# Optimization experiments

Hardware: AMD Instinct MI355X
Metric: run time of the kernel (lower is better)

Reference implementation:

```python
import jax, jax.numpy as jnp
import numpy as np
from jax import lax

BETA = 0.5        # Sinkhron beta
N_ITER = 20       # got_iteration
THRESH = 0.1      # P > 0.1 threshold
NL_I = 5          # apply_non_linearity(..., 'elu', i=5)
EPS = 1e-9


def setup_inputs() -> dict:
    key = jax.random.key(0)
    k1, k2 = jax.random.split(key)
    B, N, D = 128, 512, 128
    h = jax.random.normal(k1, (B, N, D), dtype=jnp.float32)
    W0 = jnp.ones((D,), dtype=jnp.float32)
    W1 = jnp.ones((D,), dtype=jnp.float32)
    lengths = jax.random.randint(k2, (B,), 0, N, dtype=jnp.int32)
    return {"h": h, "W0": W0, "W1": W1, "lengths": lengths}


def _forward(h, W0, W1, lengths):
    B, N, D = h.shape
    lengths = jnp.maximum(lengths, 1)
    mask = (jnp.arange(N)[None, :] < lengths[:, None])          # [B, N] bool
    mf = mask.astype(h.dtype)
    mask2 = mf[:, :, None] * mf[:, None, :]                      # [B, N, N]

    # internal_forward: Diag layers with relu between (mlp_act='relu')
    h = h * W0
    h = jax.nn.relu(h)
    h = h * W1

    # cost_matrix_batch_torch: cosine similarity, add identity diag, mask
    hn = h / (jnp.linalg.norm(h, axis=-1, keepdims=True) + 1e-12)
    sim = jnp.einsum('bnd,bmd->bnm', hn, hn)                     # [B, N, N]
    sim = sim + jnp.eye(N, dtype=h.dtype)                        # add_eye_diag
    sim = sim * mask2
    cost = (1.0 - sim) * mask2

    # Sinkhorn with uniform marginals on valid nodes, fixed iterations
    n = lengths.astype(h.dtype)
    mu = mf / n[:, None]                                         # [B, N]
    K = jnp.exp(-cost / BETA) * mask2                            # [B, N, N]

    def body(carry, _):
        u, v = carry
        u = mu / (jnp.einsum('bnm,bm->bn', K, v) + EPS) * mf
        v = mu / (jnp.einsum('bnm,bn->bm', K, u) + EPS) * mf
        return (u, v), None

    (u, v), _ = lax.scan(body, (mf, mf), None, length=N_ITER)
    P = u[:, :, None] * K * v[:, None, :]                        # transport plan

    # P.detach(); scale by number of nodes per graph; threshold
    P = lax.stop_gradient(P)
    P = n[:, None, None] * P
    A = (P > THRESH).astype(h.dtype)
    similarity = A * sim
    # apply_non_linearity 'elu': elu(x*i - i) + 1
    out = jax.nn.elu(similarity * NL_I - NL_I) + 1.0
    return out


def reference(h, W0, W1, lengths):
    return _forward(h, W0, W1, lengths)
```

## Files before the change

kernel.cpp:

```cpp
#include <hip/hip_runtime.h>

#define BB 128
#define NN 512
#define DD 128

__global__ __launch_bounds__(256) void hn_kernel(const float* __restrict__ h,
                                                 const float* __restrict__ W0,
                                                 const float* __restrict__ W1,
                                                 float* __restrict__ hn) {
    int wave = (int)((blockIdx.x * blockDim.x + threadIdx.x) >> 6);
    int lane = threadIdx.x & 63;
    const float2* h2 = (const float2*)(h + (size_t)wave * DD);
    float2 w0 = ((const float2*)W0)[lane];
    float2 w1 = ((const float2*)W1)[lane];
    float2 x = h2[lane];
    float p0 = fmaxf(x.x * w0.x, 0.0f) * w1.x;
    float p1 = fmaxf(x.y * w0.y, 0.0f) * w1.y;
    float ss = p0 * p0 + p1 * p1;
#pragma unroll
    for (int m = 32; m; m >>= 1) ss += __shfl_xor(ss, m);
    float inv = 1.0f / (sqrtf(ss) + 1e-12f);
    float2 o;
    o.x = p0 * inv;
    o.y = p1 * inv;
    ((float2*)(hn + (size_t)wave * DD))[lane] = o;
}

#define KC 32
__global__ __launch_bounds__(256) void sim_kernel(const float* __restrict__ hn,
                                                  const int* __restrict__ lengths,
                                                  float* __restrict__ K) {
    __shared__ float As[KC][132];
    __shared__ float Bs[KC][132];
    __shared__ int pre[BB + 1];
    int tid = threadIdx.x;
    if (tid == 0) {
        int acc = 0;
        for (int b = 0; b < BB; b++) {
            pre[b] = acc;
            int len = max(lengths[b], 1);
            int nt = (len + 127) >> 7;
            acc += nt * nt;
        }
        pre[BB] = acc;
    }
    __syncthreads();
    int total = pre[BB];

    int lr = tid >> 3;
    int lk = (tid & 7) << 2;
    int tx = tid & 15, ty = tid >> 4;

    for (int t = blockIdx.x; t < total; t += gridDim.x) {
        int lo = 0, hi = BB;
        while (lo + 1 < hi) {
            int mid = (lo + hi) >> 1;
            if (pre[mid] <= t) lo = mid; else hi = mid;
        }
        int b = lo;
        int local = t - pre[b];
        int len = max(lengths[b], 1);
        int nt = (len + 127) >> 7;
        int ti = local / nt;
        int tj = local - ti * nt;
        int r0 = ti << 7, c0 = tj << 7;
        const float* base = hn + (size_t)b * NN * DD;
        float acc[8][8] = {};

        for (int kc = 0; kc < DD; kc += KC) {
#pragma unroll
            for (int rr = 0; rr < 128; rr += 32) {
                float4 a = *(const float4*)(base + (size_t)(r0 + lr + rr) * DD + kc + lk);
                As[lk + 0][lr + rr] = a.x; As[lk + 1][lr + rr] = a.y;
                As[lk + 2][lr + rr] = a.z; As[lk + 3][lr + rr] = a.w;
                float4 bb = *(const float4*)(base + (size_t)(c0 + lr + rr) * DD + kc + lk);
                Bs[lk + 0][lr + rr] = bb.x; Bs[lk + 1][lr + rr] = bb.y;
                Bs[lk + 2][lr + rr] = bb.z; Bs[lk + 3][lr + rr] = bb.w;
            }
            __syncthreads();
#pragma unroll
            for (int kk = 0; kk < KC; kk++) {
                float4 a0 = *(const float4*)&As[kk][ty * 8];
                float4 a1 = *(const float4*)&As[kk][ty * 8 + 4];
                float4 b0 = *(const float4*)&Bs[kk][tx * 4];
                float4 b1 = *(const float4*)&Bs[kk][64 + tx * 4];
                float ar[8] = {a0.x, a0.y, a0.z, a0.w, a1.x, a1.y, a1.z, a1.w};
                float bc[8] = {b0.x, b0.y, b0.z, b0.w, b1.x, b1.y, b1.z, b1.w};
#pragma unroll
                for (int r = 0; r < 8; r++)
#pragma unroll
                    for (int c = 0; c < 8; c++)
                        acc[r][c] = fmaf(ar[r], bc[c], acc[r][c]);
            }
            __syncthreads();
        }
        float* out = K + (size_t)b * NN * NN;
#pragma unroll
        for (int r = 0; r < 8; r++) {
            int i = r0 + ty * 8 + r;
            if (i >= len) continue;
#pragma unroll
            for (int cg = 0; cg < 2; cg++) {
                int j0 = c0 + cg * 64 + tx * 4;
                if (j0 >= len) continue;
                float vv[4];
#pragma unroll
                for (int c = 0; c < 4; c++) {
                    float s = acc[r][cg * 4 + c] + ((i == j0 + c) ? 1.0f : 0.0f);
                    vv[c] = expf(2.0f * s - 2.0f);
                }
                float4 o;
                o.x = vv[0]; o.y = vv[1]; o.z = vv[2]; o.w = vv[3];
                *(float4*)(out + (size_t)i * NN + j0) = o;
            }
        }
    }
}

__device__ __forceinline__ float dot8(float4 A, float4 B, float4 x0, float4 x1) {
    float d = fmaf(A.x, x0.x, fmaf(A.y, x0.y, fmaf(A.z, x0.z, A.w * x0.w)));
    return fmaf(B.x, x1.x, fmaf(B.y, x1.y, fmaf(B.z, x1.z, fmaf(B.w, x1.w, d))));
}

#define ROWS22(X) X(0) X(1) X(2) X(3) X(4) X(5) X(6) X(7) X(8) X(9) X(10) \
    X(11) X(12) X(13) X(14) X(15) X(16) X(17) X(18) X(19) X(20) X(21)

__global__ __launch_bounds__(512, 2) void coop_sink(const float* __restrict__ K,
                                                    float* __restrict__ u_buf,
                                                    float* __restrict__ v_buf,
                                                    const int* __restrict__ lengths,
                                                    unsigned long long* __restrict__ slots64) {
    __shared__ float xb[NN];
    __shared__ float pv[8 * NN];
    __shared__ int Sh[BB], Pre[BB];

    int g = blockIdx.x;
    int tid = threadIdx.x;

    if (tid == 0) {
        int need[BB]; int ssum = 0;
        for (int m = 0; m < BB; m++) {
            int L = max(lengths[m], 1);
            need[m] = (L + 175) / 176;
            ssum += need[m];
        }
        while (ssum > 256) {
            int best = 0, bv = need[0];
            for (int m = 1; m < BB; m++)
                if (need[m] > bv) { bv = need[m]; best = m; }
            need[best]--; ssum--;
        }
        int acc = 0;
        for (int m = 0; m < BB; m++) { Pre[m] = acc; Sh[m] = need[m]; acc += need[m]; }
    }
    __syncthreads();

    int m = -1;
    for (int mm = 0; mm < BB; mm++)
        if (g >= Pre[mm] && g < Pre[mm] + Sh[mm]) { m = mm; break; }
    if (m < 0) return;
    int b = m;
    int jbase = Pre[m];
    int q = g - jbase;
    int S = Sh[m];

    int len = max(lengths[b], 1);
    int len4 = (len + 3) & ~3;
    int rpq = (len + S - 1) / S;
    int r_lo = q * rpq;
    int nrows = min(len - r_lo, rpq);
    if (nrows < 0) nrows = 0;
    float inv_n = 1.0f / (float)len;

    int w = tid >> 6, l = tid & 63;
    int c0 = 4 * l, c1 = 256 + 4 * l;
    bool a0 = c0 < len4, a1 = c1 < len4;
    const float* Kb = K + (size_t)b * NN * NN;

    xb[tid] = (tid < len) ? 1.0f : 0.0f;

#define DECL(o) float4 kA##o = {0,0,0,0}, kB##o = {0,0,0,0};
    ROWS22(DECL)
#undef DECL
#define FILL_ROW(o)                                                          \
    {                                                                        \
        int i_ = w + 8 * (o);                                                \
        if (i_ < nrows) {                                                    \
            const float* g0_ = Kb + (size_t)(r_lo + i_) * NN;                \
            if (a0) kA##o = *(const float4*)(g0_ + c0);                      \
            if (a1) kB##o = *(const float4*)(g0_ + c1);                      \
        }                                                                    \
    }
    ROWS22(FILL_ROW)
#undef FILL_ROW

    __syncthreads();

    for (int t = 0; t < 20; t++) {
        float4 xv0 = *(const float4*)(xb + c0);
        float4 xv1 = *(const float4*)(xb + c1);
        float4 pa = {0, 0, 0, 0}, pb = {0, 0, 0, 0};

#define DOT(o) float d##o = dot8(kA##o, kB##o, xv0, xv1);
        ROWS22(DOT)
#undef DOT
#pragma unroll
        for (int mm2 = 32; mm2; mm2 >>= 1) {
#define BF(o) d##o += __shfl_xor(d##o, mm2);
            ROWS22(BF)
#undef BF
        }
#define RC(o) float uu##o = inv_n / (d##o + 1e-9f);
        ROWS22(RC)
#undef RC
#define ACC_ROW(o)                                                           \
    pa.x = fmaf(kA##o.x, uu##o, pa.x); pa.y = fmaf(kA##o.y, uu##o, pa.y);    \
    pa.z = fmaf(kA##o.z, uu##o, pa.z); pa.w = fmaf(kA##o.w, uu##o, pa.w);    \
    pb.x = fmaf(kB##o.x, uu##o, pb.x); pb.y = fmaf(kB##o.y, uu##o, pb.y);    \
    pb.z = fmaf(kB##o.z, uu##o, pb.z); pb.w = fmaf(kB##o.w, uu##o, pb.w);
        ROWS22(ACC_ROW)
#undef ACC_ROW
        if (t == 19 && l == 0) {
            float* ub = u_buf + (size_t)b * NN + r_lo + w;
#define ST(o) if (w + 8 * (o) < nrows) ub[8 * (o)] = uu##o;
            ROWS22(ST)
#undef ST
        }

        for (int i = 176 + w; i < nrows; i += 8) {
            const float* g0 = Kb + (size_t)(r_lo + i) * NN;
            float4 A = {0, 0, 0, 0}, B = {0, 0, 0, 0};
            if (a0) A = *(const float4*)(g0 + c0);
            if (a1) B = *(const float4*)(g0 + c1);
            float d = dot8(A, B, xv0, xv1);
#pragma unroll
            for (int mm2 = 32; mm2; mm2 >>= 1) d += __shfl_xor(d, mm2);
            float uu = inv_n / (d + 1e-9f);
            pa.x = fmaf(A.x, uu, pa.x); pa.y = fmaf(A.y, uu, pa.y);
            pa.z = fmaf(A.z, uu, pa.z); pa.w = fmaf(A.w, uu, pa.w);
            pb.x = fmaf(B.x, uu, pb.x); pb.y = fmaf(B.y, uu, pb.y);
            pb.z = fmaf(B.z, uu, pb.z); pb.w = fmaf(B.w, uu, pb.w);
            if (t == 19 && l == 0) u_buf[(size_t)b * NN + r_lo + i] = uu;
        }

        *(float4*)(pv + w * NN + c0) = pa;
        *(float4*)(pv + w * NN + c1) = pb;
        __syncthreads();
        int c = tid;
        float s0 = pv[c] + pv[NN + c] + pv[2 * NN + c] + pv[3 * NN + c] +
                   pv[4 * NN + c] + pv[5 * NN + c] + pv[6 * NN + c] + pv[7 * NN + c];
        unsigned long long* pbase =
            slots64 + ((size_t)(t & 1) * 512) * 512;
        if (S > 1) {
            unsigned long long pk =
                ((unsigned long long)(unsigned)(t + 1) << 32) | __float_as_uint(s0);
            __hip_atomic_store(pbase + (size_t)g * 512 + c, pk,
                               __ATOMIC_RELAXED, __HIP_MEMORY_SCOPE_AGENT);
        }

        float t0 = s0;
        for (int s = 1; s < S; s++) {
            int k = q + s; if (k >= S) k -= S;
            const unsigned long long* p64 = pbase + (size_t)(jbase + k) * 512 + c;
            unsigned long long vpk =
                __hip_atomic_load(p64, __ATOMIC_RELAXED, __HIP_MEMORY_SCOPE_AGENT);
            while ((unsigned)(vpk >> 32) != (unsigned)(t + 1)) {
                __builtin_amdgcn_s_sleep(1);
                vpk = __hip_atomic_load(p64, __ATOMIC_RELAXED, __HIP_MEMORY_SCOPE_AGENT);
            }
            t0 += __uint_as_float((unsigned)vpk);
        }
        float v0 = (c < len) ? (inv_n / (t0 + 1e-9f)) : 0.0f;
        if (t < 19) {
            xb[c] = v0;
        } else if (c >= r_lo && c < r_lo + nrows) {
            v_buf[(size_t)b * NN + c] = v0;
        }
        __syncthreads();
    }
}

__global__ __launch_bounds__(256) void epi_kernel(float* __restrict__ io,
                                                  const float* __restrict__ u,
                                                  const float* __restrict__ v,
                                                  const int* __restrict__ lengths) {
    const float E5 = 0.006737946999085467f;
    size_t idx = (size_t)blockIdx.x * 256 + threadIdx.x;
    int b = (int)(idx >> 16);
    int r = (int)(idx >> 7) & (NN - 1);
    int c4 = ((int)idx & 127) << 2;
    int len = max(lengths[b], 1);
    float4 o;
    if (r >= len || c4 >= len) {
        o.x = E5; o.y = E5; o.z = E5; o.w = E5;
        ((float4*)io)[idx] = o;
        return;
    }
    float4 k = ((float4*)io)[idx];
    float ui = u[(size_t)b * NN + r];
    float4 vv = *(const float4*)(v + (size_t)b * NN + c4);
    float t = (float)len * ui;
    float kv[4] = {k.x, k.y, k.z, k.w};
    float vj[4] = {vv.x, vv.y, vv.z, vv.w};
    float ov[4];
#pragma unroll
    for (int c = 0; c < 4; c++) {
        float Kc = kv[c];
        float P = t * Kc * vj[c];
        bool valid = (c4 + c) < len;
        if (valid && P > 0.1f) {
            float x = 2.5f * logf(Kc);
            ov[c] = (x > 0.0f) ? (x + 1.0f) : expf(x);
        } else {
            ov[c] = E5;
        }
    }
    o.x = ov[0]; o.y = ov[1]; o.z = ov[2]; o.w = ov[3];
    ((float4*)io)[idx] = o;
}

extern "C" void kernel_launch(void* const* d_in, const int* in_sizes, int n_in,
                              void* d_out, int out_size, void* d_ws, size_t ws_size,
                              hipStream_t stream) {
    const float* h = (const float*)d_in[0];
    const float* W0 = (const float*)d_in[1];
    const float* W1 = (const float*)d_in[2];
    const int* lengths = (const int*)d_in[3];
    float* K = (float*)d_out;

    char* ws = (char*)d_ws;
    float* hn = (float*)ws;
    size_t off = (size_t)BB * NN * DD * 4;
    float* u = (float*)(ws + off); off += (size_t)BB * NN * 4;
    float* v = (float*)(ws + off); off += (size_t)BB * NN * 4;
    unsigned long long* slots64 = (unsigned long long*)(ws + off);
    off += (size_t)2 * 512 * 512 * 8;

    hn_kernel<<<BB * NN / 4, 256, 0, stream>>>(h, W0, W1, hn);
    sim_kernel<<<1024, 256, 0, stream>>>(hn, lengths, K);

    coop_sink<<<256, 512, 0, stream>>>(K, u, v, lengths, slots64);

    epi_kernel<<<(unsigned)((size_t)BB * NN * NN / 4 / 256), 256, 0, stream>>>(K, u, v, lengths);
}
```

Before: 362.6 us.

## Exploit symmetry of similarity matrix by computing only upper-triangular tiles

The sim kernel now enumerates only tiles with ti <= tj per batch, about halving the GEMM work. For each off-diagonal tile it transposes the accumulator through shared memory and writes the mirrored exp(K) block as well. This removes redundant dot products, at the cost of extra shared-memory traffic, additional barriers and a small loop to decode the tile index.

```diff
diff --git a/kernel.cpp b/kernel.cpp
--- a/kernel.cpp
+++ b/kernel.cpp
@@ -40,7 +40,7 @@
             pre[b] = acc;
             int len = max(lengths[b], 1);
             int nt = (len + 127) >> 7;
-            acc += nt * nt;
+            acc += nt * (nt + 1) / 2;
         }
         pre[BB] = acc;
     }
@@ -61,8 +61,9 @@
         int local = t - pre[b];
         int len = max(lengths[b], 1);
         int nt = (len + 127) >> 7;
-        int ti = local / nt;
-        int tj = local - ti * nt;
+        int ti = 0, rem = local;
+        while (rem >= nt - ti) { rem -= nt - ti; ti++; }
+        int tj = ti + rem;
         int r0 = ti << 7, c0 = tj << 7;
         const float* base = hn + (size_t)b * NN * DD;
         float acc[8][8] = {};
@@ -113,6 +114,42 @@
                 o.x = vv[0]; o.y = vv[1]; o.z = vv[2]; o.w = vv[3];
                 *(float4*)(out + (size_t)i * NN + j0) = o;
             }
+        }
+        if (ti != tj) {
+#pragma unroll
+            for (int cg = 0; cg < 2; cg++) {
+                for (int half = 0; half < 2; half++) {
+                    __syncthreads();
+                    if ((tx >> 3) == half) {
+                        int jl = (tx & 7) * 4;
+#pragma unroll
+                        for (int r = 0; r < 8; r++)
+#pragma unroll
+                            for (int c = 0; c < 4; c++)
+                                As[jl + c][ty * 8 + r] = acc[r][cg * 4 + c];
+                    }
+                    __syncthreads();
+                    int jrow = tid >> 3;
+                    int j = c0 + cg * 64 + half * 32 + jrow;
+                    if (j < len) {
+                        int ib = (tid & 7) * 16;
+#pragma unroll
+                        for (int s4 = 0; s4 < 4; s4++) {
+                            int il = ib + s4 * 4;
+                            int i0 = r0 + il;
+                            if (i0 >= len) continue;
+                            float4 sraw = *(const float4*)&As[jrow][il];
+                            float4 o;
+                            o.x = expf(2.0f * sraw.x - 2.0f);
+                            o.y = expf(2.0f * sraw.y - 2.0f);
+                            o.z = expf(2.0f * sraw.z - 2.0f);
+                            o.w = expf(2.0f * sraw.w - 2.0f);
+                            *(float4*)(out + (size_t)j * NN + i0) = o;
+                        }
+                    }
+                }
+            }
+            __syncthreads();
         }
     }
 }
```

Measured after the change: 358.5 us (median of 3 runs). No clear change (-1.1%).
